# Optimization experiments

Hardware: AMD Instinct MI355X
Metric: run time of the kernel (lower is better)

The kernel has to match this reference:

```python
import jax, jax.numpy as jnp
import numpy as np

B, D, H, O, E = 8192, 1024, 4096, 1024, 3

def setup_inputs() -> dict:
    key = jax.random.key(0)
    ks = jax.random.split(key, 8)
    s = lambda fan_in: 1.0 / np.sqrt(fan_in)
    return {
        "x":   jax.random.normal(ks[0], (B, D), jnp.float32),
        "gw1": jax.random.normal(ks[1], (D, 256), jnp.float32) * s(D),
        "gb1": jnp.zeros((256,), jnp.float32),
        "gw2": jax.random.normal(ks[2], (256, 128), jnp.float32) * s(256),
        "gb2": jnp.zeros((128,), jnp.float32),
        "gw3": jax.random.normal(ks[3], (128, E), jnp.float32) * s(128),
        "gb3": jnp.zeros((E,), jnp.float32),
        "ew1": jax.random.normal(ks[4], (E, D, H), jnp.float32) * s(D),
        "eb1": jnp.zeros((E, H), jnp.float32),
        "ew2": jax.random.normal(ks[5], (E, H, O), jnp.float32) * s(H),
        "eb2": jnp.zeros((E, O), jnp.float32),
        "top_k": 2,
    }

def reference(x, gw1, gb1, gw2, gb2, gw3, gb3, ew1, eb1, ew2, eb2, top_k):
    # Gating network (dropout is identity in eval mode)
    g = jax.nn.relu(x @ gw1 + gb1)
    g = jax.nn.relu(g @ gw2 + gb2)
    gates = jax.nn.softmax(g @ gw3 + gb3, axis=-1)          # [B, E]

    # top-k routing with renormalized weights
    topk_scores, topk_idx = jax.lax.top_k(gates, top_k)     # [B, k]
    topk_scores = topk_scores / jnp.sum(topk_scores, axis=-1, keepdims=True)

    # scatter normalized scores into dense [B, E] combine weights
    b_ix = jnp.arange(x.shape[0])[:, None]
    combine = jnp.zeros_like(gates).at[b_ix, topk_idx].add(topk_scores)  # [B, E]

    # run all experts densely (small E=3), combine with routing weights
    eh = jax.nn.relu(jnp.einsum('bd,edh->beh', x, ew1) + eb1[None])      # [B, E, H]
    eo = jnp.einsum('beh,eho->beo', eh, ew2) + eb2[None]                 # [B, E, O]
    out = jnp.einsum('be,beo->bo', combine, eo)                          # [B, O]
    return out, gates
```

## Files before the change

kernel.cpp:

```cpp
#include <hip/hip_runtime.h>
#include <cstdint>
#include <cstddef>

#define B_ROWS 8192
#define D_DIM  1024
#define H_DIM  4096
#define O_DIM  1024
#define E_NUM  3
#define K2     (2 * H_DIM)
#define MT_MAX 66
#define SLOT_MAX (MT_MAX * 128)

typedef __attribute__((ext_vector_type(4))) float f4;
typedef __attribute__((ext_vector_type(8))) _Float16 half8;

__device__ __forceinline__ unsigned short f2h_bits(float f) {
  _Float16 h = (_Float16)f;
  return __builtin_bit_cast(unsigned short, h);
}

__device__ __forceinline__ void async16(const void* g, void* l) {
  __builtin_amdgcn_global_load_lds(
      (const __attribute__((address_space(1))) unsigned int*)g,
      (__attribute__((address_space(3))) unsigned int*)l, 16, 0, 0);
}

__global__ __launch_bounds__(256) void k_cast_x(const float* __restrict__ in,
                                                unsigned short* __restrict__ out) {
  size_t i = (size_t)blockIdx.x * 256 + threadIdx.x;
  const f4* p = (const f4*)in;
  f4 a = p[2 * i], b = p[2 * i + 1];
  half8 h;
#pragma unroll
  for (int j = 0; j < 4; ++j) { h[j] = (_Float16)a[j]; h[4 + j] = (_Float16)b[j]; }
  *(half8*)(out + 8 * i) = h;
}

__global__ __launch_bounds__(256) void k_transpose_cast(const float* __restrict__ in,
                                                        unsigned short* __restrict__ out,
                                                        int R, int C) {
  __shared__ float tile[32][33];
  const size_t eoff = (size_t)blockIdx.z * R * C;
  const float* I = in + eoff;
  unsigned short* O = out + eoff;
  int c0 = blockIdx.x * 32, r0 = blockIdx.y * 32;
  int tx = threadIdx.x & 31, ty = threadIdx.x >> 5;
#pragma unroll
  for (int i = 0; i < 4; ++i)
    tile[ty + 8 * i][tx] = I[(size_t)(r0 + ty + 8 * i) * C + c0 + tx];
  __syncthreads();
#pragma unroll
  for (int i = 0; i < 4; ++i)
    O[(size_t)(c0 + ty + 8 * i) * R + r0 + tx] = f2h_bits(tile[tx][ty + 8 * i]);
}

__global__ __launch_bounds__(256) void k_gemm_f32(const float* __restrict__ A,
                                                  const float* __restrict__ Bm,
                                                  const float* __restrict__ bias,
                                                  float* __restrict__ C,
                                                  int N, int K) {
  __shared__ float sAT[16][68];
  __shared__ float sB[16][68];
  const int t = threadIdx.x;
  const int tx = t & 15, ty = t >> 4;
  const int m0 = blockIdx.y * 64, n0 = blockIdx.x * 64;
  float acc[4][4] = {};
  for (int k0 = 0; k0 < K; k0 += 16) {
    __syncthreads();
#pragma unroll
    for (int i = 0; i < 4; ++i) {
      int idx = t + i * 256;
      int r = idx >> 4, c = idx & 15;
      sAT[c][r] = A[(size_t)(m0 + r) * K + (k0 + c)];
      int rb = idx >> 6, cb = idx & 63;
      sB[rb][cb] = Bm[(size_t)(k0 + rb) * N + (n0 + cb)];
    }
    __syncthreads();
#pragma unroll
    for (int kk = 0; kk < 16; ++kk) {
      f4 av = *(const f4*)&sAT[kk][ty * 4];
      f4 bv = *(const f4*)&sB[kk][tx * 4];
#pragma unroll
      for (int i = 0; i < 4; ++i)
#pragma unroll
        for (int j = 0; j < 4; ++j)
          acc[i][j] = fmaf(av[i], bv[j], acc[i][j]);
    }
  }
#pragma unroll
  for (int i = 0; i < 4; ++i) {
    int row = m0 + ty * 4 + i;
    f4 v;
#pragma unroll
    for (int j = 0; j < 4; ++j)
      v[j] = fmaxf(acc[i][j] + bias[n0 + tx * 4 + j], 0.f);
    *(f4*)&C[(size_t)row * N + n0 + tx * 4] = v;
  }
}

__global__ __launch_bounds__(256) void k_gate_topk(const float* __restrict__ h2,
                                                   const float* __restrict__ gw3,
                                                   const float* __restrict__ gb3,
                                                   float* __restrict__ gates,
                                                   float* __restrict__ combine,
                                                   int* __restrict__ bucket) {
  const int lane = threadIdx.x & 63;
  const int row = blockIdx.x * 4 + (threadIdx.x >> 6);
  const float* h = h2 + (size_t)row * 128;
  float h0 = h[lane], h1 = h[lane + 64];
  float l0 = h0 * gw3[lane * 3 + 0] + h1 * gw3[(lane + 64) * 3 + 0];
  float l1 = h0 * gw3[lane * 3 + 1] + h1 * gw3[(lane + 64) * 3 + 1];
  float l2 = h0 * gw3[lane * 3 + 2] + h1 * gw3[(lane + 64) * 3 + 2];
#pragma unroll
  for (int off = 32; off > 0; off >>= 1) {
    l0 += __shfl_down(l0, off);
    l1 += __shfl_down(l1, off);
    l2 += __shfl_down(l2, off);
  }
  if (lane == 0) {
    float g0 = l0 + gb3[0], g1v = l1 + gb3[1], g2v = l2 + gb3[2];
    float mx = fmaxf(g0, fmaxf(g1v, g2v));
    float e0 = expf(g0 - mx), e1 = expf(g1v - mx), e2 = expf(g2v - mx);
    float inv = 1.f / (e0 + e1 + e2);
    float p0 = e0 * inv, p1 = e1 * inv, p2 = e2 * inv;
    gates[row * 3 + 0] = p0; gates[row * 3 + 1] = p1; gates[row * 3 + 2] = p2;
    int amin = 0; float pm = p0;
    if (p1 <= pm) { pm = p1; amin = 1; }
    if (p2 <= pm) { pm = p2; amin = 2; }
    float denom = (p0 + p1 + p2) - pm;
    combine[row * 3 + 0] = (amin == 0) ? 0.f : p0 / denom;
    combine[row * 3 + 1] = (amin == 1) ? 0.f : p1 / denom;
    combine[row * 3 + 2] = (amin == 2) ? 0.f : p2 / denom;
    bucket[row] = amin;
  }
}

__global__ __launch_bounds__(256) void k_count(const int* __restrict__ bucket,
                                               int* __restrict__ cnt) {
  int row = blockIdx.x * 256 + threadIdx.x;
  int b = bucket[row];
  int lane = threadIdx.x & 63;
#pragma unroll
  for (int bid = 0; bid < 3; ++bid) {
    unsigned long long m = __ballot(b == bid);
    if (m && b == bid) {
      int prefix = __popcll(m & ((1ull << lane) - 1));
      if (prefix == 0) atomicAdd(&cnt[bid], __popcll(m));
    }
  }
}

__global__ void k_meta(const int* __restrict__ cnt, int* __restrict__ meta,
                       int* __restrict__ cnt2) {
  int t0 = (cnt[0] + 127) >> 7;
  int t1 = (cnt[1] + 127) >> 7;
  int t2 = (cnt[2] + 127) >> 7;
  meta[0] = 0; meta[1] = t0; meta[2] = t0 + t1; meta[3] = t0 + t1 + t2;
  cnt2[0] = 0; cnt2[1] = 0; cnt2[2] = 0;
}

__global__ __launch_bounds__(256) void k_scatter(const int* __restrict__ bucket,
                                                 const int* __restrict__ meta,
                                                 int* __restrict__ cnt2,
                                                 int* __restrict__ sorted) {
  int row = blockIdx.x * 256 + threadIdx.x;
  int b = bucket[row];
  int lane = threadIdx.x & 63;
#pragma unroll
  for (int bid = 0; bid < 3; ++bid) {
    unsigned long long m = __ballot(b == bid);
    if (m) {
      int cntm = __popcll(m);
      int leader = __ffsll((unsigned long long)m) - 1;
      int base = 0;
      if (lane == leader) base = atomicAdd(&cnt2[bid], cntm);
      base = __shfl(base, leader);
      if (b == bid) {
        int prefix = __popcll(m & ((1ull << lane) - 1));
        sorted[meta[bid] * 128 + base + prefix] = row;
      }
    }
  }
}

__device__ __forceinline__ void bucket_experts(int b, int& ea, int& eb) {
  ea = (b == 0) ? 1 : 0;
  eb = (b == 2) ? 1 : 2;
}

__global__ __launch_bounds__(256) void k_expert_h(const unsigned short* __restrict__ Xh,
                                                  const unsigned short* __restrict__ W1T,
                                                  const float* __restrict__ combine,
                                                  const float* __restrict__ eb1,
                                                  const int* __restrict__ sorted,
                                                  const int* __restrict__ meta,
                                                  unsigned short* __restrict__ EHS) {
  constexpr int K = D_DIM;
  const int lin = blockIdx.x;
  const int group = lin / (MT_MAX * 4);
  const int rem = lin % (MT_MAX * 4);
  const int mt = rem % MT_MAX;
  const int nb = group * 4 + rem / MT_MAX;
  const int tb1 = meta[1], tb2 = meta[2], tb3 = meta[3];
  if (mt >= tb3) return;
  const int b = (mt >= tb2) ? 2 : (mt >= tb1) ? 1 : 0;
  int ea, ebx; bucket_experts(b, ea, ebx);
  const int z = blockIdx.z;
  const int e = z ? ebx : ea;
  const int slot0 = mt * 128;
  const int n0 = nb * 128;

  __shared__ __align__(16) char smem[32768];
  __shared__ float sC[128];
  char* sA = smem;
  char* sB = smem + 16384;
  const int t = threadIdx.x;
  if (t < 128) {
    int r = sorted[slot0 + t];
    sC[t] = (r < 0) ? 0.f : combine[(size_t)r * 3 + e];
  }

  const unsigned short* aptr[4];
  const unsigned short* bptr[4];
  int soff[4];
#pragma unroll
  for (int i = 0; i < 4; ++i) {
    int sa = t + i * 256;
    int row = sa >> 3;
    int j = (sa & 7) ^ (row & 7);
    soff[i] = sa * 16;
    int r = sorted[slot0 + row];
    int rr = (r < 0) ? 0 : r;
    aptr[i] = Xh + (size_t)rr * K + j * 8;
    bptr[i] = W1T + (size_t)e * H_DIM * K + (size_t)(n0 + row) * K + j * 8;
  }
  const int lane = t & 63;
  const int wm = (t >> 6) & 1, wn = t >> 7;
  const int quad = lane >> 4, l16 = lane & 15;
  int offA[4][2], offB[4][2];
#pragma unroll
  for (int mtile = 0; mtile < 4; ++mtile) {
    int ra = wm * 64 + mtile * 16 + l16;
    int rb = wn * 64 + mtile * 16 + l16;
#pragma unroll
    for (int s = 0; s < 2; ++s) {
      offA[mtile][s] = ra * 128 + (((s * 4 + quad) ^ (ra & 7)) * 16);
      offB[mtile][s] = rb * 128 + (((s * 4 + quad) ^ (rb & 7)) * 16);
    }
  }
  f4 acc[4][4] = {};
  for (int k0 = 0; k0 < K; k0 += 64) {
#pragma unroll
    for (int i = 0; i < 4; ++i) {
      async16(aptr[i] + k0, sA + soff[i]);
      async16(bptr[i] + k0, sB + soff[i]);
    }
    __syncthreads();
#pragma unroll
    for (int s = 0; s < 2; ++s) {
      half8 a[4], bfr[4];
#pragma unroll
      for (int i = 0; i < 4; ++i) a[i] = *(const half8*)(sA + offA[i][s]);
#pragma unroll
      for (int i = 0; i < 4; ++i) bfr[i] = *(const half8*)(sB + offB[i][s]);
#pragma unroll
      for (int i = 0; i < 4; ++i)
#pragma unroll
        for (int jn = 0; jn < 4; ++jn)
          acc[i][jn] = __builtin_amdgcn_mfma_f32_16x16x32_f16(a[i], bfr[jn], acc[i][jn], 0, 0, 0);
    }
    __syncthreads();
  }
  const float* bias = eb1 + (size_t)e * H_DIM;
#pragma unroll
  for (int nt = 0; nt < 4; ++nt) {
    int col = n0 + wn * 64 + nt * 16 + l16;
    float bb = bias[col];
#pragma unroll
    for (int mtile = 0; mtile < 4; ++mtile) {
#pragma unroll
      for (int r = 0; r < 4; ++r) {
        int rloc = wm * 64 + mtile * 16 + quad * 4 + r;
        float v = fmaxf(acc[mtile][nt][r] + bb, 0.f) * sC[rloc];
        EHS[(size_t)(slot0 + rloc) * K2 + (size_t)z * H_DIM + col] = f2h_bits(v);
      }
    }
  }
}

__global__ __launch_bounds__(256) void k_expert_o(const unsigned short* __restrict__ EHS,
                                                  const unsigned short* __restrict__ W2T,
                                                  const float* __restrict__ combine,
                                                  const float* __restrict__ eb2,
                                                  const int* __restrict__ sorted,
                                                  const int* __restrict__ meta,
                                                  float* __restrict__ OUT) {
  const int mt = blockIdx.y;
  const int tb1 = meta[1], tb2 = meta[2], tb3 = meta[3];
  if (mt >= tb3) return;
  const int b = (mt >= tb2) ? 2 : (mt >= tb1) ? 1 : 0;
  int ea, ebx; bucket_experts(b, ea, ebx);
  const int z = blockIdx.z;
  const int e = z ? ebx : ea;
  const int slot0 = mt * 128;
  const int n0 = blockIdx.x * 128;

  __shared__ __align__(16) char smem[32768];
  __shared__ int sRow[128];
  __shared__ float sC[128];
  char* sA = smem;
  char* sB = smem + 16384;
  const int t = threadIdx.x;
  if (t < 128) {
    int r = sorted[slot0 + t];
    sRow[t] = r;
    sC[t] = (r < 0) ? 0.f : combine[(size_t)r * 3 + e];
  }

  const unsigned short* ap[4];
  const unsigned short* bp[4];
  int soff[4];
  const unsigned short* Ab = EHS + (size_t)slot0 * K2 + (size_t)z * H_DIM;
  const unsigned short* Bb = W2T + (size_t)e * O_DIM * H_DIM + (size_t)n0 * H_DIM;
#pragma unroll
  for (int i = 0; i < 4; ++i) {
    int sa = t + i * 256;
    int row = sa >> 3;
    int j = (sa & 7) ^ (row & 7);
    soff[i] = sa * 16;
    ap[i] = Ab + (size_t)row * K2 + j * 8;
    bp[i] = Bb + (size_t)row * H_DIM + j * 8;
  }
  const int lane = t & 63;
  const int wm = (t >> 6) & 1, wn = t >> 7;
  const int quad = lane >> 4, l16 = lane & 15;
  int offA[4][2], offB[4][2];
#pragma unroll
  for (int mtile = 0; mtile < 4; ++mtile) {
    int ra = wm * 64 + mtile * 16 + l16;
    int rb = wn * 64 + mtile * 16 + l16;
#pragma unroll
    for (int s = 0; s < 2; ++s) {
      offA[mtile][s] = ra * 128 + (((s * 4 + quad) ^ (ra & 7)) * 16);
      offB[mtile][s] = rb * 128 + (((s * 4 + quad) ^ (rb & 7)) * 16);
    }
  }
  f4 acc[4][4] = {};
  for (int k0 = 0; k0 < H_DIM; k0 += 64) {
#pragma unroll
    for (int i = 0; i < 4; ++i) {
      async16(ap[i] + k0, sA + soff[i]);
      async16(bp[i] + k0, sB + soff[i]);
    }
    __syncthreads();
#pragma unroll
    for (int s = 0; s < 2; ++s) {
      half8 a[4], bfr[4];
#pragma unroll
      for (int i = 0; i < 4; ++i) a[i] = *(const half8*)(sA + offA[i][s]);
#pragma unroll
      for (int i = 0; i < 4; ++i) bfr[i] = *(const half8*)(sB + offB[i][s]);
#pragma unroll
      for (int i = 0; i < 4; ++i)
#pragma unroll
        for (int jn = 0; jn < 4; ++jn)
          acc[i][jn] = __builtin_amdgcn_mfma_f32_16x16x32_f16(a[i], bfr[jn], acc[i][jn], 0, 0, 0);
    }
    __syncthreads();
  }
#pragma unroll
  for (int nt = 0; nt < 4; ++nt) {
    int col = n0 + wn * 64 + nt * 16 + l16;
    float be = eb2[(size_t)e * O_DIM + col];
#pragma unroll
    for (int mtile = 0; mtile < 4; ++mtile) {
#pragma unroll
      for (int r = 0; r < 4; ++r) {
        int rloc = wm * 64 + mtile * 16 + quad * 4 + r;
        int rowg = sRow[rloc];
        if (rowg >= 0) {
          float v = acc[mtile][nt][r] + sC[rloc] * be;
          atomicAdd(&OUT[(size_t)rowg * O_DIM + col], v);
        }
      }
    }
  }
}

extern "C" void kernel_launch(void* const* d_in, const int* in_sizes, int n_in,
                              void* d_out, int out_size, void* d_ws, size_t ws_size,
                              hipStream_t stream) {
  const float* x   = (const float*)d_in[0];
  const float* gw1 = (const float*)d_in[1];
  const float* gb1 = (const float*)d_in[2];
  const float* gw2 = (const float*)d_in[3];
  const float* gb2 = (const float*)d_in[4];
  const float* gw3 = (const float*)d_in[5];
  const float* gb3 = (const float*)d_in[6];
  const float* ew1 = (const float*)d_in[7];
  const float* eb1 = (const float*)d_in[8];
  const float* ew2 = (const float*)d_in[9];
  const float* eb2 = (const float*)d_in[10];
  float* out = (float*)d_out;
  float* gates = out + (size_t)B_ROWS * O_DIM;

  char* ws = (char*)d_ws;
  size_t off = 0;
  auto take = [&](size_t bytes) -> char* {
    char* p = ws + off;
    off += (bytes + 255) & ~(size_t)255;
    return p;
  };
  unsigned short* xh  = (unsigned short*)take((size_t)B_ROWS * D_DIM * 2);
  unsigned short* w1t = (unsigned short*)take((size_t)E_NUM * H_DIM * D_DIM * 2);
  unsigned short* w2t = (unsigned short*)take((size_t)E_NUM * O_DIM * H_DIM * 2);
  float* comb   = (float*)take((size_t)B_ROWS * 3 * 4);
  float* g1     = (float*)take((size_t)B_ROWS * 256 * 4);
  float* h2     = (float*)take((size_t)B_ROWS * 128 * 4);
  int* bucket   = (int*)take((size_t)B_ROWS * 4);
  int* sorted   = (int*)take((size_t)SLOT_MAX * 4);
  int* cnt      = (int*)take(3 * 4);
  int* cnt2     = (int*)take(3 * 4);
  int* meta     = (int*)take(4 * 4);
  unsigned short* ehs = (unsigned short*)take((size_t)SLOT_MAX * K2 * 2);

  hipMemsetAsync(cnt, 0, 3 * 4, stream);
  hipMemsetAsync(sorted, 0xFF, (size_t)SLOT_MAX * 4, stream);
  hipMemsetAsync(out, 0, (size_t)B_ROWS * O_DIM * 4, stream);

  k_cast_x<<<dim3(B_ROWS * D_DIM / (256 * 8)), 256, 0, stream>>>(x, xh);
  k_transpose_cast<<<dim3(H_DIM / 32, D_DIM / 32, E_NUM), 256, 0, stream>>>(ew1, w1t, D_DIM, H_DIM);
  k_transpose_cast<<<dim3(O_DIM / 32, H_DIM / 32, E_NUM), 256, 0, stream>>>(ew2, w2t, H_DIM, O_DIM);

  k_gemm_f32<<<dim3(256 / 64, B_ROWS / 64), 256, 0, stream>>>(x, gw1, gb1, g1, 256, D_DIM);
  k_gemm_f32<<<dim3(128 / 64, B_ROWS / 64), 256, 0, stream>>>(g1, gw2, gb2, h2, 128, 256);
  k_gate_topk<<<dim3(B_ROWS / 4), 256, 0, stream>>>(h2, gw3, gb3, gates, comb, bucket);

  k_count<<<dim3(B_ROWS / 256), 256, 0, stream>>>(bucket, cnt);
  k_meta<<<1, 1, 0, stream>>>(cnt, meta, cnt2);
  k_scatter<<<dim3(B_ROWS / 256), 256, 0, stream>>>(bucket, meta, cnt2, sorted);

  k_expert_h<<<dim3(MT_MAX * 32, 1, 2), 256, 0, stream>>>(
      xh, w1t, comb, eb1, sorted, meta, ehs);
  k_expert_o<<<dim3(O_DIM / 128, MT_MAX, 2), 256, 0, stream>>>(
      ehs, w2t, comb, eb2, sorted, meta, out);
}
```

Baseline: 853.8 us.

## Chunk expert GEMMs over row tiles and remap blocks for XCD-local reuse

The expert H and O kernels are now launched twice, each time over half of the row tiles, alternating H then O per chunk. The intent is to keep the intermediate EHS data for a chunk resident in cache before the O GEMM reads it. Block indices are remapped so that all blocks sharing one row tile land on the same XCD (lin & 7), which should improve L2 reuse of the A operand. The trade-off is an extra pair of launches, tail imbalance within each chunk, and some blocks in padded grids that exit early.

```diff
diff --git a/kernel.cpp b/kernel.cpp
--- a/kernel.cpp
+++ b/kernel.cpp
@@ -9,6 +9,7 @@
 #define E_NUM  3
 #define K2     (2 * H_DIM)
 #define MT_MAX 66
+#define MT_CHUNK 33
 #define SLOT_MAX (MT_MAX * 128)
 
 typedef __attribute__((ext_vector_type(4))) float f4;
@@ -194,18 +195,23 @@
                                                   const float* __restrict__ eb1,
                                                   const int* __restrict__ sorted,
                                                   const int* __restrict__ meta,
-                                                  unsigned short* __restrict__ EHS) {
+                                                  unsigned short* __restrict__ EHS,
+                                                  int mt0, int mtN) {
   constexpr int K = D_DIM;
   const int lin = blockIdx.x;
-  const int group = lin / (MT_MAX * 4);
-  const int rem = lin % (MT_MAX * 4);
-  const int mt = rem % MT_MAX;
-  const int nb = group * 4 + rem / MT_MAX;
+  const int xcd = lin & 7;
+  const int rest = lin >> 3;
+  const int inner = rest & 63;
+  const int mtH = rest >> 6;
+  const int l = xcd + 8 * mtH;
+  if (l >= mtN) return;
+  const int mt = mt0 + l;
   const int tb1 = meta[1], tb2 = meta[2], tb3 = meta[3];
   if (mt >= tb3) return;
   const int b = (mt >= tb2) ? 2 : (mt >= tb1) ? 1 : 0;
   int ea, ebx; bucket_experts(b, ea, ebx);
-  const int z = blockIdx.z;
+  const int nb = inner & 31;
+  const int z = inner >> 5;
   const int e = z ? ebx : ea;
   const int slot0 = mt * 128;
   const int n0 = nb * 128;
@@ -294,16 +300,25 @@
                                                   const float* __restrict__ eb2,
                                                   const int* __restrict__ sorted,
                                                   const int* __restrict__ meta,
-                                                  float* __restrict__ OUT) {
-  const int mt = blockIdx.y;
+                                                  float* __restrict__ OUT,
+                                                  int mt0, int mtN) {
+  const int lin = blockIdx.x;
+  const int xcd = lin & 7;
+  const int rest = lin >> 3;
+  const int n = rest & 7;
+  const int gH = rest >> 3;
+  const int gl = xcd + 8 * gH;
+  if (gl >= 2 * mtN) return;
+  const int l = gl >> 1;
+  const int z = gl & 1;
+  const int mt = mt0 + l;
   const int tb1 = meta[1], tb2 = meta[2], tb3 = meta[3];
   if (mt >= tb3) return;
   const int b = (mt >= tb2) ? 2 : (mt >= tb1) ? 1 : 0;
   int ea, ebx; bucket_experts(b, ea, ebx);
-  const int z = blockIdx.z;
   const int e = z ? ebx : ea;
   const int slot0 = mt * 128;
-  const int n0 = blockIdx.x * 128;
+  const int n0 = n * 128;
 
   __shared__ __align__(16) char smem[32768];
   __shared__ int sRow[128];
@@ -440,8 +455,11 @@
   k_meta<<<1, 1, 0, stream>>>(cnt, meta, cnt2);
   k_scatter<<<dim3(B_ROWS / 256), 256, 0, stream>>>(bucket, meta, cnt2, sorted);
 
-  k_expert_h<<<dim3(MT_MAX * 32, 1, 2), 256, 0, stream>>>(
-      xh, w1t, comb, eb1, sorted, meta, ehs);
-  k_expert_o<<<dim3(O_DIM / 128, MT_MAX, 2), 256, 0, stream>>>(
-      ehs, w2t, comb, eb2, sorted, meta, out);
-}
+  const int gh = 8 * 64 * ((MT_CHUNK + 7) / 8);
+  const int go = 8 * 8 * ((2 * MT_CHUNK + 7) / 8);
+  for (int c = 0; c < 2; ++c) {
+    int mt0 = c * MT_CHUNK;
+    k_expert_h<<<dim3(gh), 256, 0, stream>>>(xh, w1t, comb, eb1, sorted, meta, ehs, mt0, MT_CHUNK);
+    k_expert_o<<<dim3(go), 256, 0, stream>>>(ehs, w2t, comb, eb2, sorted, meta, out, mt0, MT_CHUNK);
+  }
+}
```

Result: slower. 919.8 us (+7.7%).
